# Kernel optimization log

Measured on AMD Instinct MI355X. Metric: run time of the kernel, lower is better.

Reference implementation:

```python
import jax, jax.numpy as jnp
import numpy as np

N_QUBITS = 8
DIM = 1 << N_QUBITS  # 256
PI = float(np.pi)

# Computational-basis bit signs: s_i = +1 for bit 0, -1 for bit 1 (Z eigenvalues).
# PennyLane convention: wire 0 is the most-significant bit.
_bits = (np.arange(DIM)[:, None] >> (N_QUBITS - 1 - np.arange(N_QUBITS))[None, :]) & 1
SIGNS = jnp.asarray(1.0 - 2.0 * _bits, dtype=jnp.float32)  # [DIM, 8]
PAIR_SIGNS = SIGNS[:, :-1] * SIGNS[:, 1:]                  # [DIM, 7]


def _mlp(x, W1, b1, W2, b2, W3, b3):
    h = jax.nn.relu(x @ W1.T + b1)
    h = jax.nn.relu(h @ W2.T + b2)
    return h @ W3.T + b3


def _embed_state(x):
    """QuantumEmbedding1 (ZZ feature map, IQP-style) on |0>^8.

    H on every wire, RZ(x_i) on wire i, then for i in 0..6:
    CNOT(i,i+1); RZ((pi-x_i)(pi-x_{i+1}), wire i+1); CNOT(i,i+1).
    The whole post-Hadamard circuit is diagonal, so the statevector has
    closed form: psi_b = 2^{-4} exp(-i/2 * phi(b)).
    x: [B, 8] -> psi: [B, 256] complex64.
    """
    single = x @ SIGNS.T                                    # [B, DIM]
    zz = (PI - x[:, :-1]) * (PI - x[:, 1:])                 # [B, 7]
    phase = single + zz @ PAIR_SIGNS.T                      # [B, DIM]
    return jnp.exp(-0.5j * phase) / 16.0                    # complex64


def _mean_rho(psi):
    B = psi.shape[0]
    return jnp.einsum('bi,bj->ij', psi, jnp.conj(psi)) / B  # [256, 256]


def setup_inputs() -> dict:
    key = jax.random.key(0)
    ks = jax.random.split(key, 8)
    B = 65536
    inp = {
        'x1': jax.random.normal(ks[0], (B, 8), dtype=jnp.float32),
        'x0': jax.random.normal(ks[1], (B, 8), dtype=jnp.float32),
        'W1': jax.random.normal(ks[2], (10, 8), dtype=jnp.float32) / np.sqrt(8.0),
        'b1': jnp.zeros((10,), dtype=jnp.float32),
        'W2': jax.random.normal(ks[3], (10, 10), dtype=jnp.float32) / np.sqrt(10.0),
        'b2': jnp.zeros((10,), dtype=jnp.float32),
        'W3': jax.random.normal(ks[4], (8, 10), dtype=jnp.float32) / np.sqrt(10.0),
        'b3': jnp.zeros((8,), dtype=jnp.float32),
    }
    return inp


def reference(x1, x0, W1, b1, W2, b2, W3, b3):
    h1 = _mlp(x1, W1, b1, W2, b2, W3, b3)
    h0 = _mlp(x0, W1, b1, W2, b2, W3, b3)
    rho1 = _mean_rho(_embed_state(h1))
    rho0 = _mean_rho(_embed_state(h0))
    rho_diff = rho1 - rho0
    rho_diff = 0.5 * (rho_diff + jnp.conj(rho_diff.T))  # exact Hermitian
    eigvals = jnp.linalg.eigvalsh(rho_diff)             # real eigenvalues
    return -0.5 * jnp.sum(jnp.abs(eigvals))
```

## Files before the change

### kernel.cpp

```cpp
#include <hip/hip_runtime.h>
#include <cstdint>
#include <cstddef>
#include <utility>

#define PI_F 3.14159265358979323846f

typedef __attribute__((ext_vector_type(8))) _Float16 half8;
typedef __attribute__((ext_vector_type(4))) float f32x4;

struct U4 { unsigned int w[4]; };

static __device__ __forceinline__ unsigned int packhalf2(float c, float s) {
  _Float16 hc = (_Float16)c, hs = (_Float16)s;
  unsigned short uc = __builtin_bit_cast(unsigned short, hc);
  unsigned short us = __builtin_bit_cast(unsigned short, hs);
  return (unsigned int)uc | ((unsigned int)us << 16);
}

static __device__ __forceinline__ void load16_lds(const void* g, void* l) {
  __builtin_amdgcn_global_load_lds(
      (const __attribute__((address_space(1))) unsigned int*)g,
      (__attribute__((address_space(3))) unsigned int*)l, 16, 0, 0);
}

__global__ __launch_bounds__(256) void k_mlp(
    const float* __restrict__ x1, const float* __restrict__ x0,
    const float* __restrict__ W1, const float* __restrict__ b1,
    const float* __restrict__ W2, const float* __restrict__ b2,
    const float* __restrict__ W3, const float* __restrict__ b3,
    float* __restrict__ hz, int B, float* __restrict__ scalars,
    float* __restrict__ out) {
  int s = blockIdx.x * blockDim.x + threadIdx.x;
  if (blockIdx.x == 0 && threadIdx.x == 0) {
    scalars[0] = 0.f;
    scalars[1] = 0.f;
    out[0] = 0.f;
  }
  if (s >= 2 * B) return;
  const float* xp = (s < B) ? (x1 + (size_t)s * 8) : (x0 + (size_t)(s - B) * 8);
  float x[8];
#pragma unroll
  for (int k = 0; k < 8; k++) x[k] = xp[k];
  float a1[10];
#pragma unroll
  for (int o = 0; o < 10; o++) {
    float v = b1[o];
#pragma unroll
    for (int k = 0; k < 8; k++) v = fmaf(W1[o * 8 + k], x[k], v);
    a1[o] = fmaxf(v, 0.f);
  }
  float a2[10];
#pragma unroll
  for (int o = 0; o < 10; o++) {
    float v = b2[o];
#pragma unroll
    for (int k = 0; k < 10; k++) v = fmaf(W2[o * 10 + k], a1[k], v);
    a2[o] = fmaxf(v, 0.f);
  }
  float h[8];
#pragma unroll
  for (int o = 0; o < 8; o++) {
    float v = b3[o];
#pragma unroll
    for (int k = 0; k < 10; k++) v = fmaf(W3[o * 10 + k], a2[k], v);
    h[o] = v;
  }
  float outv[16];
#pragma unroll
  for (int k = 0; k < 8; k++) outv[k] = h[k];
#pragma unroll
  for (int k = 0; k < 7; k++) outv[8 + k] = (PI_F - h[k]) * (PI_F - h[k + 1]);
  outv[15] = 0.f;
  float4* dst = (float4*)(hz + (size_t)s * 16);
#pragma unroll
  for (int q = 0; q < 4; q++) dst[q] = ((float4*)outv)[q];
}

__global__ __launch_bounds__(256) void k_gen(const float* __restrict__ hz,
                                             _Float16* __restrict__ Ach) {
  __shared__ float hzl[32][17];
  int kb = blockIdx.x, t = threadIdx.x;
  if (t < 128) {
    int smp = t >> 2, q = t & 3;
    const float4 v =
        *(const float4*)(hz + (size_t)(kb * 32 + smp) * 16 + q * 4);
    hzl[smp][q * 4 + 0] = v.x;
    hzl[smp][q * 4 + 1] = v.y;
    hzl[smp][q * 4 + 2] = v.z;
    hzl[smp][q * 4 + 3] = v.w;
  }
  __syncthreads();
  int s = t & 31, oct = t >> 5;
  float h[8], z[7];
#pragma unroll
  for (int k = 0; k < 8; k++) h[k] = hzl[s][k];
#pragma unroll
  for (int k = 0; k < 7; k++) z[k] = hzl[s][8 + k];
  float S5 = (oct & 4) ? -1.f : 1.f;
  float S6 = (oct & 2) ? -1.f : 1.f;
  float S7 = (oct & 1) ? -1.f : 1.f;
  float sg[5] = {1.f, 1.f, 1.f, 1.f, 1.f};
  float phi = h[0] + h[1] + h[2] + h[3] + h[4] + S5 * h[5] + S6 * h[6] +
              S7 * h[7] + z[0] + z[1] + z[2] + z[3] + S5 * z[4] +
              S5 * S6 * z[5] + S6 * S7 * z[6];
  _Float16* dst = Ach + (size_t)kb * 16384;
  const int halfoff = (2 * s) ^ (oct << 3);

  auto emit = [&](int g, float ph) {
    float r = ph * 0.07957747154594767f;
    r = r - floorf(r);
    float sv = __builtin_amdgcn_sinf(r);
    float cv = __builtin_amdgcn_cosf(r);
    *(unsigned int*)(dst + (size_t)(g * 8 + oct) * 64 + halfoff) =
        packhalf2(cv, sv);
  };

  emit(0, phi);
#pragma unroll
  for (int jj = 1; jj < 32; ++jj) {
    const int b = __builtin_ctz(jj);
    const int w = 4 - b;
    float nbl = (w == 0) ? 0.f : sg[w - 1] * z[w - 1];
    float nbr = (w == 4) ? S5 * z[4] : sg[w + 1] * z[w];
    phi -= 2.f * sg[w] * (h[w] + nbl + nbr);
    sg[w] = -sg[w];
    emit(jj ^ (jj >> 1), phi);
  }
}

#define ZSLABS 256

__global__ __launch_bounds__(256) void k_gemm(const _Float16* __restrict__ A,
                                              float* __restrict__ P,
                                              int kbPer) {
  __shared__ _Float16 lds[2][2][128][64];
  int bx = blockIdx.x, z = blockIdx.y;
  bool diag = (bx < 2);
  int mbase = (bx == 2) ? 0 : bx * 128;
  int nbase = (bx == 0) ? 0 : 128;
  int tile = (bx == 2) ? 1 : bx * 2;
  int bp = diag ? 0 : 1;
  int t = threadIdx.x, wave = t >> 6, lane = t & 63;
  int wm = wave >> 1, wn = wave & 1;
  unsigned int reMask = (z < ZSLABS / 2) ? 0u : 0x80008000u;
  unsigned int imMask = (z < ZSLABS / 2) ? 0x80000000u : 0x00008000u;
  int kb0 = z * kbPer;

  auto stage = [&](int it, int buf) {
    size_t kb = (size_t)(kb0 + it);
    const char* gA = (const char*)A + kb * 32768 + (size_t)mbase * 128;
    char* lA = (char*)&lds[buf][0][0][0];
#pragma unroll
    for (int q = 0; q < 4; q++) {
      int woff = wave * 4096 + q * 1024;
      load16_lds(gA + woff + lane * 16, lA + woff);
    }
    if (!diag) {
      const char* gB = (const char*)A + kb * 32768 + (size_t)nbase * 128;
      char* lB = (char*)&lds[buf][1][0][0];
#pragma unroll
      for (int q = 0; q < 4; q++) {
        int woff = wave * 4096 + q * 1024;
        load16_lds(gB + woff + lane * 16, lB + woff);
      }
    }
  };

  f32x4 accR[4][4] = {};
  f32x4 accI[4][4] = {};
  stage(0, 0);
  for (int it = 0; it < kbPer; ++it) {
    __syncthreads();
    if (it + 1 < kbPer) stage(it + 1, (it + 1) & 1);
    int buf = it & 1;
#pragma unroll
    for (int kk = 0; kk < 2; kk++) {
      int cbase = kk * 4 + (lane >> 4);
      half8 af[4], bfr[4], bfi[4];
#pragma unroll
      for (int fm = 0; fm < 4; fm++) {
        int r = wm * 64 + fm * 16 + (lane & 15);
        af[fm] = *(const half8*)&lds[buf][0][r][(cbase ^ (r & 7)) << 3];
      }
#pragma unroll
      for (int fn = 0; fn < 4; fn++) {
        int r = wn * 64 + fn * 16 + (lane & 15);
        half8 bv = *(const half8*)&lds[buf][bp][r][(cbase ^ (r & 7)) << 3];
        U4 u = __builtin_bit_cast(U4, bv), ur, ui;
#pragma unroll
        for (int q = 0; q < 4; q++) {
          unsigned int xv = u.w[q];
          ur.w[q] = xv ^ reMask;
          ui.w[q] = ((xv << 16) | (xv >> 16)) ^ imMask;
        }
        bfr[fn] = __builtin_bit_cast(half8, ur);
        bfi[fn] = __builtin_bit_cast(half8, ui);
      }
#pragma unroll
      for (int fm = 0; fm < 4; fm++)
#pragma unroll
        for (int fn = 0; fn < 4; fn++) {
          accR[fm][fn] = __builtin_amdgcn_mfma_f32_16x16x32_f16(
              af[fm], bfr[fn], accR[fm][fn], 0, 0, 0);
          accI[fm][fn] = __builtin_amdgcn_mfma_f32_16x16x32_f16(
              af[fm], bfi[fn], accI[fm][fn], 0, 0, 0);
        }
    }
  }
  float* PR = P + ((size_t)(tile * ZSLABS + z) * 2) * 16384;
  float* PI = PR + 16384;
  int r4 = (lane >> 4) * 4, cj = lane & 15;
#pragma unroll
  for (int fm = 0; fm < 4; fm++)
#pragma unroll
    for (int fn = 0; fn < 4; fn++)
#pragma unroll
      for (int r = 0; r < 4; r++) {
        int li = wm * 64 + fm * 16 + r4 + r;
        int lj = wn * 64 + fn * 16 + cj;
        PR[li * 128 + lj] = accR[fm][fn][r];
        PI[li * 128 + lj] = accI[fm][fn][r];
      }
}

__global__ __launch_bounds__(128) void k_reduce1(const float* __restrict__ P,
                                                 float* __restrict__ Q) {
  int r = blockIdx.x, tile = blockIdx.y, g = blockIdx.z, c = threadIdx.x;
  const float* base =
      P + ((size_t)(tile * ZSLABS + g * 32) * 2) * 16384 + r * 128 + c;
  float vR = 0.f, vI = 0.f;
  for (int u = 0; u < 32; u++) {
    vR += base[(size_t)u * 32768];
    vI += base[(size_t)u * 32768 + 16384];
  }
  size_t qidx = ((size_t)(g * 3 + tile) * 128 + r) * 128 + c;
  Q[qidx] = vR;
  Q[qidx + (size_t)8 * 3 * 16384] = vI;
}

__global__ __launch_bounds__(128) void k_reduce2(const float* __restrict__ Q,
                                                 float* __restrict__ AR,
                                                 float* __restrict__ AI,
                                                 float* __restrict__ sumsq,
                                                 float scale) {
  int r = blockIdx.x, tile = blockIdx.y, c = threadIdx.x;
  float vR = 0.f, vI = 0.f;
#pragma unroll
  for (int g = 0; g < 8; g++) {
    size_t qidx = ((size_t)(g * 3 + tile) * 128 + r) * 128 + c;
    vR += Q[qidx];
    vI += Q[qidx + (size_t)8 * 3 * 16384];
  }
  vR *= scale;
  vI *= scale;
  int i = (tile == 2) ? 128 + r : r;
  int j = (tile == 0) ? c : 128 + c;
  float ss = 0.f;
  bool diagTile = (tile != 1);
  if (!diagTile || c > r) {
    AR[i * 256 + j] = vR;
    AR[j * 256 + i] = vR;
    AI[i * 256 + j] = vI;
    AI[j * 256 + i] = -vI;
    ss = 2.f * (vR * vR + vI * vI);
  } else if (c == r) {
    AR[i * 256 + j] = vR;
    AI[i * 256 + j] = 0.f;
    ss = vR * vR;
  }
#pragma unroll
  for (int o = 32; o > 0; o >>= 1) ss += __shfl_down(ss, o);
  __shared__ float w2[2];
  if ((c & 63) == 0) w2[c >> 6] = ss;
  __syncthreads();
  if (c == 0) atomicAdd(sumsq, w2[0] + w2[1]);
}

__global__ __launch_bounds__(1024) void k_csq(
    const float* __restrict__ XR, const float* __restrict__ XI,
    float* __restrict__ YR, float* __restrict__ YI,
    float* __restrict__ sumsqY, int accumNorm) {
  __shared__ float rp[16][256][2];
  __shared__ float cpT[16][258][2];
  __shared__ float pacc[3][256][2];
  __shared__ float w16[16];
  int t = threadIdx.x;
  int bi = blockIdx.x >> 4, bj = blockIdx.x & 15;
  {
    int r = t >> 6, c = (t & 63) * 4;
    const float4 vr = *(const float4*)&XR[(bi * 16 + r) * 256 + c];
    const float4 vi = *(const float4*)&XI[(bi * 16 + r) * 256 + c];
    rp[r][c + 0][0] = vr.x; rp[r][c + 1][0] = vr.y;
    rp[r][c + 2][0] = vr.z; rp[r][c + 3][0] = vr.w;
    rp[r][c + 0][1] = vi.x; rp[r][c + 1][1] = vi.y;
    rp[r][c + 2][1] = vi.z; rp[r][c + 3][1] = vi.w;
    int row = t >> 2, c0 = (t & 3) * 4;
    const float4 wr = *(const float4*)&XR[row * 256 + bj * 16 + c0];
    const float4 wi = *(const float4*)&XI[row * 256 + bj * 16 + c0];
    cpT[c0 + 0][row][0] = wr.x; cpT[c0 + 1][row][0] = wr.y;
    cpT[c0 + 2][row][0] = wr.z; cpT[c0 + 3][row][0] = wr.w;
    cpT[c0 + 0][row][1] = wi.x; cpT[c0 + 1][row][1] = wi.y;
    cpT[c0 + 2][row][1] = wi.z; cpT[c0 + 3][row][1] = wi.w;
  }
  __syncthreads();
  int sub = t >> 8, tt = t & 255, ty = tt >> 4, tx = tt & 15;
  float sR = 0.f, sI = 0.f;
  int k0 = sub * 64;
#pragma unroll 8
  for (int k = k0; k < k0 + 64; k++) {
    float xr = rp[ty][k][0], xi = rp[ty][k][1];
    float yr = cpT[tx][k][0], yi = cpT[tx][k][1];
    sR = fmaf(xr, yr, sR);
    sR = fmaf(-xi, yi, sR);
    sI = fmaf(xr, yi, sI);
    sI = fmaf(xi, yr, sI);
  }
  if (sub) {
    pacc[sub - 1][tt][0] = sR;
    pacc[sub - 1][tt][1] = sI;
  }
  __syncthreads();
  float v = 0.f;
  if (sub == 0) {
    sR += (pacc[0][tt][0] + pacc[1][tt][0]) + pacc[2][tt][0];
    sI += (pacc[0][tt][1] + pacc[1][tt][1]) + pacc[2][tt][1];
    int i = bi * 16 + ty, j = bj * 16 + tx;
    YR[i * 256 + j] = sR;
    YI[i * 256 + j] = sI;
    if (accumNorm) v = sR * sR + sI * sI;
  }
#pragma unroll
  for (int o = 32; o > 0; o >>= 1) v += __shfl_down(v, o);
  if ((t & 63) == 0) w16[t >> 6] = v;
  __syncthreads();
  if (t == 0 && accumNorm)
    atomicAdd(sumsqY, (w16[0] + w16[1]) + (w16[2] + w16[3]));
}

__global__ __launch_bounds__(1024) void k_cupd(
    const float* __restrict__ XR, const float* __restrict__ XI,
    const float* __restrict__ YR, const float* __restrict__ YI,
    float* __restrict__ ZR, float* __restrict__ ZI,
    const float* __restrict__ scalars, int mode,
    const float* __restrict__ AR, const float* __restrict__ AI,
    float* __restrict__ out, int finalTrace) {
  __shared__ float rp[16][256][2];
  __shared__ float cpT[16][258][2];
  __shared__ float pacc[3][256][2];
  __shared__ float w16[16];
  int t = threadIdx.x;
  int bi = blockIdx.x >> 4, bj = blockIdx.x & 15;
  {
    int r = t >> 6, c = (t & 63) * 4;
    const float4 vr = *(const float4*)&XR[(bi * 16 + r) * 256 + c];
    const float4 vi = *(const float4*)&XI[(bi * 16 + r) * 256 + c];
    rp[r][c + 0][0] = vr.x; rp[r][c + 1][0] = vr.y;
    rp[r][c + 2][0] = vr.z; rp[r][c + 3][0] = vr.w;
    rp[r][c + 0][1] = vi.x; rp[r][c + 1][1] = vi.y;
    rp[r][c + 2][1] = vi.z; rp[r][c + 3][1] = vi.w;
    int row = t >> 2, c0 = (t & 3) * 4;
    const float4 wr = *(const float4*)&YR[row * 256 + bj * 16 + c0];
    const float4 wi = *(const float4*)&YI[row * 256 + bj * 16 + c0];
    cpT[c0 + 0][row][0] = wr.x; cpT[c0 + 1][row][0] = wr.y;
    cpT[c0 + 2][row][0] = wr.z; cpT[c0 + 3][row][0] = wr.w;
    cpT[c0 + 0][row][1] = wi.x; cpT[c0 + 1][row][1] = wi.y;
    cpT[c0 + 2][row][1] = wi.z; cpT[c0 + 3][row][1] = wi.w;
  }
  __syncthreads();
  int sub = t >> 8, tt = t & 255, ty = tt >> 4, tx = tt & 15;
  float sR = 0.f, sI = 0.f;
  int k0 = sub * 64;
#pragma unroll 8
  for (int k = k0; k < k0 + 64; k++) {
    float xr = rp[ty][k][0], xi = rp[ty][k][1];
    float yr = cpT[tx][k][0], yi = cpT[tx][k][1];
    sR = fmaf(xr, yr, sR);
    sR = fmaf(-xi, yi, sR);
    sI = fmaf(xr, yi, sI);
    sI = fmaf(xi, yr, sI);
  }
  if (sub) {
    pacc[sub - 1][tt][0] = sR;
    pacc[sub - 1][tt][1] = sI;
  }
  __syncthreads();
  float v = 0.f;
  if (sub == 0) {
    sR += (pacc[0][tt][0] + pacc[1][tt][0]) + pacc[2][tt][0];
    sI += (pacc[0][tt][1] + pacc[1][tt][1]) + pacc[2][tt][1];
    float aC, bC;
    if (mode == 0) {
      float f2 = scalars[0];
      float f = sqrtf(f2);
      float Rhat = 1.41421356f * sqrtf(scalars[1]) / f2;
      float g = 1.0f / (1.75f * Rhat);
      aC = 1.5f * g / f;
      float gf = g / f;
      bC = 0.5f * gf * gf * gf;
    } else if (mode == 1) {
      aC = 2.0f;
      bC = 1.0f;
    } else {
      aC = 1.5f;
      bC = 0.5f;
    }
    int idx = (bi * 16 + ty) * 256 + bj * 16 + tx;
    float zr = aC * XR[idx] - bC * sR;
    float zi = aC * XI[idx] - bC * sI;
    if (!finalTrace) {
      ZR[idx] = zr;
      ZI[idx] = zi;
    } else {
      v = AR[idx] * zr + AI[idx] * zi;
    }
  }
#pragma unroll
  for (int o = 32; o > 0; o >>= 1) v += __shfl_down(v, o);
  if ((t & 63) == 0) w16[t >> 6] = v;
  __syncthreads();
  if (t == 0 && finalTrace)
    atomicAdd(out, -0.5f * ((w16[0] + w16[1]) + (w16[2] + w16[3])));
}

extern "C" void kernel_launch(void* const* d_in, const int* in_sizes, int n_in,
                              void* d_out, int out_size, void* d_ws,
                              size_t ws_size, hipStream_t stream) {
  const float* x1 = (const float*)d_in[0];
  const float* x0 = (const float*)d_in[1];
  const float* W1 = (const float*)d_in[2];
  const float* b1 = (const float*)d_in[3];
  const float* W2 = (const float*)d_in[4];
  const float* b2 = (const float*)d_in[5];
  const float* W3 = (const float*)d_in[6];
  const float* b3 = (const float*)d_in[7];
  (void)n_in;
  (void)out_size;
  (void)ws_size;

  const int B = in_sizes[0] / 8;
  const int total = 2 * B;
  const int totalKb = total / 32;
  const int kbPer = totalKb / ZSLABS;

  char* ws = (char*)d_ws;
  size_t off = 0;
  auto carve = [&](size_t bytes) -> void* {
    off = (off + 255) & ~(size_t)255;
    void* p = ws + off;
    off += bytes;
    return p;
  };
  float* hz = (float*)carve((size_t)total * 16 * 4);
  _Float16* Ach = (_Float16*)carve((size_t)totalKb * 16384 * 2);
  float* P = (float*)carve((size_t)3 * ZSLABS * 2 * 16384 * 4);
  float* Q = (float*)carve((size_t)2 * 8 * 3 * 16384 * 4);
  float* scalars = (float*)carve(256);
  float* AR = (float*)carve(256 * 256 * 4);
  float* AI = (float*)carve(256 * 256 * 4);
  float* XR = (float*)carve(256 * 256 * 4);
  float* XI = (float*)carve(256 * 256 * 4);
  float* YR = (float*)carve(256 * 256 * 4);
  float* YI = (float*)carve(256 * 256 * 4);
  float* ZR = (float*)carve(256 * 256 * 4);
  float* ZI = (float*)carve(256 * 256 * 4);

  k_mlp<<<(total + 255) / 256, 256, 0, stream>>>(
      x1, x0, W1, b1, W2, b2, W3, b3, hz, B, scalars, (float*)d_out);
  k_gen<<<totalKb, 256, 0, stream>>>(hz, Ach);
  k_gemm<<<dim3(3, ZSLABS), 256, 0, stream>>>(Ach, P, kbPer);
  k_reduce1<<<dim3(128, 3, 8), 128, 0, stream>>>(P, Q);
  k_reduce2<<<dim3(128, 3), 128, 0, stream>>>(Q, AR, AI, scalars,
                                              1.0f / (256.0f * (float)B));

  const int NIT = 11;
  float *cR = AR, *cI = AI, *nR = XR, *nI = XI;
  for (int it = 0; it < NIT; it++) {
    int mode = (it == 0) ? 0 : (it <= 6 ? 1 : 2);
    int fin = (it == NIT - 1) ? 1 : 0;
    k_csq<<<256, 1024, 0, stream>>>(cR, cI, YR, YI, scalars + 1, it == 0);
    k_cupd<<<256, 1024, 0, stream>>>(cR, cI, YR, YI, nR, nI, scalars, mode, AR,
                                     AI, (float*)d_out, fin);
    if (it == 0) {
      cR = XR; cI = XI; nR = ZR; nI = ZI;
    } else {
      std::swap(cR, nR);
      std::swap(cI, nI);
    }
  }
}
```

Before: 264.8 us.

## Fuse Newton-Schulz iterations into one cooperative persistent kernel with grid sync

Replaces the 22 separate k_csq/k_cupd launches of the 11-iteration Newton-Schulz sign loop with a single cooperative kernel. The kernel runs all iterations and separates the dependent phases with grid.sync(). It also reuses the row panel already staged in shared memory for the aC*X term instead of re-reading X from global. The aim is to remove per-launch overhead and gaps between launches. In exchange it adds grid-wide barrier costs and requires all 256 blocks of 1024 threads to be co-resident.

New measurement: 896.6 us. 239% more time.

```diff
diff --git a/kernel.cpp b/kernel.cpp
--- a/kernel.cpp
+++ b/kernel.cpp
@@ -1,7 +1,10 @@
 #include <hip/hip_runtime.h>
+#include <hip/hip_cooperative_groups.h>
 #include <cstdint>
 #include <cstddef>
 #include <utility>
+
+namespace cg = cooperative_groups;
 
 #define PI_F 3.14159265358979323846f
 
@@ -276,119 +279,93 @@
   if (c == 0) atomicAdd(sumsq, w2[0] + w2[1]);
 }
 
-__global__ __launch_bounds__(1024) void k_csq(
-    const float* __restrict__ XR, const float* __restrict__ XI,
-    float* __restrict__ YR, float* __restrict__ YI,
-    float* __restrict__ sumsqY, int accumNorm) {
+__global__ __launch_bounds__(1024) void k_ns(
+    const float* AR, const float* AI, float* XR, float* XI, float* YR,
+    float* YI, float* ZR, float* ZI, float* scalars, float* out, int NIT) {
+  cg::grid_group grid = cg::this_grid();
   __shared__ float rp[16][256][2];
   __shared__ float cpT[16][258][2];
   __shared__ float pacc[3][256][2];
   __shared__ float w16[16];
-  int t = threadIdx.x;
-  int bi = blockIdx.x >> 4, bj = blockIdx.x & 15;
-  {
-    int r = t >> 6, c = (t & 63) * 4;
-    const float4 vr = *(const float4*)&XR[(bi * 16 + r) * 256 + c];
-    const float4 vi = *(const float4*)&XI[(bi * 16 + r) * 256 + c];
-    rp[r][c + 0][0] = vr.x; rp[r][c + 1][0] = vr.y;
-    rp[r][c + 2][0] = vr.z; rp[r][c + 3][0] = vr.w;
-    rp[r][c + 0][1] = vi.x; rp[r][c + 1][1] = vi.y;
-    rp[r][c + 2][1] = vi.z; rp[r][c + 3][1] = vi.w;
-    int row = t >> 2, c0 = (t & 3) * 4;
-    const float4 wr = *(const float4*)&XR[row * 256 + bj * 16 + c0];
-    const float4 wi = *(const float4*)&XI[row * 256 + bj * 16 + c0];
-    cpT[c0 + 0][row][0] = wr.x; cpT[c0 + 1][row][0] = wr.y;
-    cpT[c0 + 2][row][0] = wr.z; cpT[c0 + 3][row][0] = wr.w;
-    cpT[c0 + 0][row][1] = wi.x; cpT[c0 + 1][row][1] = wi.y;
-    cpT[c0 + 2][row][1] = wi.z; cpT[c0 + 3][row][1] = wi.w;
-  }
-  __syncthreads();
-  int sub = t >> 8, tt = t & 255, ty = tt >> 4, tx = tt & 15;
-  float sR = 0.f, sI = 0.f;
-  int k0 = sub * 64;
+  const int t = threadIdx.x;
+  const int bi = blockIdx.x >> 4, bj = blockIdx.x & 15;
+  const int sub = t >> 8, tt = t & 255, ty = tt >> 4, tx = tt & 15;
+  const int idx = (bi * 16 + ty) * 256 + bj * 16 + tx;
+
+  auto MM = [&](const float* LRr, const float* LIi, const float* RRr,
+                const float* RIi, float& sR, float& sI) {
+    __syncthreads();
+    {
+      int r = t >> 6, c = (t & 63) * 4;
+      const float4 vr = *(const float4*)&LRr[(bi * 16 + r) * 256 + c];
+      const float4 vi = *(const float4*)&LIi[(bi * 16 + r) * 256 + c];
+      rp[r][c + 0][0] = vr.x; rp[r][c + 1][0] = vr.y;
+      rp[r][c + 2][0] = vr.z; rp[r][c + 3][0] = vr.w;
+      rp[r][c + 0][1] = vi.x; rp[r][c + 1][1] = vi.y;
+      rp[r][c + 2][1] = vi.z; rp[r][c + 3][1] = vi.w;
+      int row = t >> 2, c0 = (t & 3) * 4;
+      const float4 wr = *(const float4*)&RRr[row * 256 + bj * 16 + c0];
+      const float4 wi = *(const float4*)&RIi[row * 256 + bj * 16 + c0];
+      cpT[c0 + 0][row][0] = wr.x; cpT[c0 + 1][row][0] = wr.y;
+      cpT[c0 + 2][row][0] = wr.z; cpT[c0 + 3][row][0] = wr.w;
+      cpT[c0 + 0][row][1] = wi.x; cpT[c0 + 1][row][1] = wi.y;
+      cpT[c0 + 2][row][1] = wi.z; cpT[c0 + 3][row][1] = wi.w;
+    }
+    __syncthreads();
+    sR = 0.f;
+    sI = 0.f;
+    int k0 = sub * 64;
 #pragma unroll 8
-  for (int k = k0; k < k0 + 64; k++) {
-    float xr = rp[ty][k][0], xi = rp[ty][k][1];
-    float yr = cpT[tx][k][0], yi = cpT[tx][k][1];
-    sR = fmaf(xr, yr, sR);
-    sR = fmaf(-xi, yi, sR);
-    sI = fmaf(xr, yi, sI);
-    sI = fmaf(xi, yr, sI);
-  }
-  if (sub) {
-    pacc[sub - 1][tt][0] = sR;
-    pacc[sub - 1][tt][1] = sI;
-  }
-  __syncthreads();
-  float v = 0.f;
-  if (sub == 0) {
-    sR += (pacc[0][tt][0] + pacc[1][tt][0]) + pacc[2][tt][0];
-    sI += (pacc[0][tt][1] + pacc[1][tt][1]) + pacc[2][tt][1];
-    int i = bi * 16 + ty, j = bj * 16 + tx;
-    YR[i * 256 + j] = sR;
-    YI[i * 256 + j] = sI;
-    if (accumNorm) v = sR * sR + sI * sI;
-  }
-#pragma unroll
-  for (int o = 32; o > 0; o >>= 1) v += __shfl_down(v, o);
-  if ((t & 63) == 0) w16[t >> 6] = v;
-  __syncthreads();
-  if (t == 0 && accumNorm)
-    atomicAdd(sumsqY, (w16[0] + w16[1]) + (w16[2] + w16[3]));
-}
-
-__global__ __launch_bounds__(1024) void k_cupd(
-    const float* __restrict__ XR, const float* __restrict__ XI,
-    const float* __restrict__ YR, const float* __restrict__ YI,
-    float* __restrict__ ZR, float* __restrict__ ZI,
-    const float* __restrict__ scalars, int mode,
-    const float* __restrict__ AR, const float* __restrict__ AI,
-    float* __restrict__ out, int finalTrace) {
-  __shared__ float rp[16][256][2];
-  __shared__ float cpT[16][258][2];
-  __shared__ float pacc[3][256][2];
-  __shared__ float w16[16];
-  int t = threadIdx.x;
-  int bi = blockIdx.x >> 4, bj = blockIdx.x & 15;
-  {
-    int r = t >> 6, c = (t & 63) * 4;
-    const float4 vr = *(const float4*)&XR[(bi * 16 + r) * 256 + c];
-    const float4 vi = *(const float4*)&XI[(bi * 16 + r) * 256 + c];
-    rp[r][c + 0][0] = vr.x; rp[r][c + 1][0] = vr.y;
-    rp[r][c + 2][0] = vr.z; rp[r][c + 3][0] = vr.w;
-    rp[r][c + 0][1] = vi.x; rp[r][c + 1][1] = vi.y;
-    rp[r][c + 2][1] = vi.z; rp[r][c + 3][1] = vi.w;
-    int row = t >> 2, c0 = (t & 3) * 4;
-    const float4 wr = *(const float4*)&YR[row * 256 + bj * 16 + c0];
-    const float4 wi = *(const float4*)&YI[row * 256 + bj * 16 + c0];
-    cpT[c0 + 0][row][0] = wr.x; cpT[c0 + 1][row][0] = wr.y;
-    cpT[c0 + 2][row][0] = wr.z; cpT[c0 + 3][row][0] = wr.w;
-    cpT[c0 + 0][row][1] = wi.x; cpT[c0 + 1][row][1] = wi.y;
-    cpT[c0 + 2][row][1] = wi.z; cpT[c0 + 3][row][1] = wi.w;
-  }
-  __syncthreads();
-  int sub = t >> 8, tt = t & 255, ty = tt >> 4, tx = tt & 15;
-  float sR = 0.f, sI = 0.f;
-  int k0 = sub * 64;
-#pragma unroll 8
-  for (int k = k0; k < k0 + 64; k++) {
-    float xr = rp[ty][k][0], xi = rp[ty][k][1];
-    float yr = cpT[tx][k][0], yi = cpT[tx][k][1];
-    sR = fmaf(xr, yr, sR);
-    sR = fmaf(-xi, yi, sR);
-    sI = fmaf(xr, yi, sI);
-    sI = fmaf(xi, yr, sI);
-  }
-  if (sub) {
-    pacc[sub - 1][tt][0] = sR;
-    pacc[sub - 1][tt][1] = sI;
-  }
-  __syncthreads();
-  float v = 0.f;
-  if (sub == 0) {
-    sR += (pacc[0][tt][0] + pacc[1][tt][0]) + pacc[2][tt][0];
-    sI += (pacc[0][tt][1] + pacc[1][tt][1]) + pacc[2][tt][1];
+    for (int k = k0; k < k0 + 64; k++) {
+      float xr = rp[ty][k][0], xi = rp[ty][k][1];
+      float yr = cpT[tx][k][0], yi = cpT[tx][k][1];
+      sR = fmaf(xr, yr, sR);
+      sR = fmaf(-xi, yi, sR);
+      sI = fmaf(xr, yi, sI);
+      sI = fmaf(xi, yr, sI);
+    }
+    if (sub) {
+      pacc[sub - 1][tt][0] = sR;
+      pacc[sub - 1][tt][1] = sI;
+    }
+    __syncthreads();
+    if (sub == 0) {
+      sR += (pacc[0][tt][0] + pacc[1][tt][0]) + pacc[2][tt][0];
+      sI += (pacc[0][tt][1] + pacc[1][tt][1]) + pacc[2][tt][1];
+    }
+  };
+
+  auto blockAtomic = [&](float v, float* dst, float scale) {
+#pragma unroll
+    for (int o = 32; o > 0; o >>= 1) v += __shfl_down(v, o);
+    if ((t & 63) == 0) w16[t >> 6] = v;
+    __syncthreads();
+    if (t == 0) {
+      float s = 0.f;
+#pragma unroll
+      for (int q = 0; q < 16; q++) s += w16[q];
+      atomicAdd(dst, scale * s);
+    }
+  };
+
+  const float *cR = AR, *cI = AI;
+  float *nR = XR, *nI = XI;
+  for (int it = 0; it < NIT; ++it) {
+    float sR, sI;
+    MM(cR, cI, cR, cI, sR, sI);
+    if (sub == 0) {
+      YR[idx] = sR;
+      YI[idx] = sI;
+    }
+    if (it == 0) {
+      float v = (sub == 0) ? (sR * sR + sI * sI) : 0.f;
+      blockAtomic(v, scalars + 1, 1.0f);
+    }
+    grid.sync();
+    float mR, mI;
+    MM(cR, cI, YR, YI, mR, mI);
     float aC, bC;
+    int mode = (it == 0) ? 0 : (it <= 6 ? 1 : 2);
     if (mode == 0) {
       float f2 = scalars[0];
       float f = sqrtf(f2);
@@ -404,22 +381,29 @@
       aC = 1.5f;
       bC = 0.5f;
     }
-    int idx = (bi * 16 + ty) * 256 + bj * 16 + tx;
-    float zr = aC * XR[idx] - bC * sR;
-    float zi = aC * XI[idx] - bC * sI;
-    if (!finalTrace) {
-      ZR[idx] = zr;
-      ZI[idx] = zi;
+    if (it < NIT - 1) {
+      if (sub == 0) {
+        nR[idx] = aC * rp[ty][bj * 16 + tx][0] - bC * mR;
+        nI[idx] = aC * rp[ty][bj * 16 + tx][1] - bC * mI;
+      }
+      grid.sync();
     } else {
-      v = AR[idx] * zr + AI[idx] * zi;
-    }
-  }
-#pragma unroll
-  for (int o = 32; o > 0; o >>= 1) v += __shfl_down(v, o);
-  if ((t & 63) == 0) w16[t >> 6] = v;
-  __syncthreads();
-  if (t == 0 && finalTrace)
-    atomicAdd(out, -0.5f * ((w16[0] + w16[1]) + (w16[2] + w16[3])));
+      float v = 0.f;
+      if (sub == 0) {
+        float zr = aC * rp[ty][bj * 16 + tx][0] - bC * mR;
+        float zi = aC * rp[ty][bj * 16 + tx][1] - bC * mI;
+        v = AR[idx] * zr + AI[idx] * zi;
+      }
+      blockAtomic(v, out, -0.5f);
+    }
+    if (it == 0) {
+      cR = XR; cI = XI; nR = ZR; nI = ZI;
+    } else {
+      const float* tmpR = cR; const float* tmpI = cI;
+      cR = nR; cI = nI;
+      nR = (float*)tmpR; nI = (float*)tmpI;
+    }
+  }
 }
 
 extern "C" void kernel_launch(void* const* d_in, const int* in_sizes, int n_in,
@@ -472,19 +456,10 @@
   k_reduce2<<<dim3(128, 3), 128, 0, stream>>>(Q, AR, AI, scalars,
                                               1.0f / (256.0f * (float)B));
 
-  const int NIT = 11;
-  float *cR = AR, *cI = AI, *nR = XR, *nI = XI;
-  for (int it = 0; it < NIT; it++) {
-    int mode = (it == 0) ? 0 : (it <= 6 ? 1 : 2);
-    int fin = (it == NIT - 1) ? 1 : 0;
-    k_csq<<<256, 1024, 0, stream>>>(cR, cI, YR, YI, scalars + 1, it == 0);
-    k_cupd<<<256, 1024, 0, stream>>>(cR, cI, YR, YI, nR, nI, scalars, mode, AR,
-                                     AI, (float*)d_out, fin);
-    if (it == 0) {
-      cR = XR; cI = XI; nR = ZR; nI = ZI;
-    } else {
-      std::swap(cR, nR);
-      std::swap(cI, nI);
-    }
-  }
-}
+  int nit = 11;
+  float* outp = (float*)d_out;
+  void* args[] = {&AR, &AI, &XR, &XI, &YR, &YI,
+                  &ZR, &ZI, &scalars, &outp, &nit};
+  hipLaunchCooperativeKernel((void*)k_ns, dim3(256), dim3(1024), args, 0,
+                             stream);
+}
```

## Restructure Hermitian GEMM into 512 load-balanced blocks with 8 waves each

Applied to the files above, without the earlier changes.

The rho GEMM kernel is replaced by one that launches 512 blocks of 512 threads. Diagonal quadrant tiles get 128 blocks with 32 k-steps each and the off-diagonal tile gets 256 blocks with 16 k-steps, so per-block work is balanced. Each wave now computes a 32x64 sub-tile with a smaller accumulator set, which is meant to raise occupancy and spread work across more CUs than the previous 3x256 grid of 4-wave blocks. The hardcoded kb0<2048 sign split and fixed slab counts tie the kernel to the batch size B=65536, and the reduction kernels are updated to index the new partial layout.

Measured after the change: 253.0 us. -4.5%, faster.

```diff
diff --git a/kernel.cpp b/kernel.cpp
--- a/kernel.cpp
+++ b/kernel.cpp
@@ -128,46 +128,33 @@
   }
 }
 
-#define ZSLABS 256
-
-__global__ __launch_bounds__(256) void k_gemm(const _Float16* __restrict__ A,
-                                              float* __restrict__ P,
-                                              int kbPer) {
-  __shared__ _Float16 lds[2][2][128][64];
-  int bx = blockIdx.x, z = blockIdx.y;
-  bool diag = (bx < 2);
-  int mbase = (bx == 2) ? 0 : bx * 128;
-  int nbase = (bx == 0) ? 0 : 128;
-  int tile = (bx == 2) ? 1 : bx * 2;
-  int bp = diag ? 0 : 1;
+__global__ __launch_bounds__(512) void k_gemm_q(const _Float16* __restrict__ A,
+                                                float* __restrict__ P) {
+  __shared__ _Float16 lds[2][16384];
+  int b = blockIdx.x;
+  int qt = (b < 128) ? 0 : (b < 384 ? 1 : 2);
+  int z = b - ((qt == 0) ? 0 : (qt == 1) ? 128 : 384);
+  int kbPer = (qt == 1) ? 16 : 32;
+  int kb0 = z * kbPer;
+  int chunkOff = (qt == 2) ? 16384 : 0;
+  int bRowBase = (qt == 1) ? 128 : 0;
   int t = threadIdx.x, wave = t >> 6, lane = t & 63;
-  int wm = wave >> 1, wn = wave & 1;
-  unsigned int reMask = (z < ZSLABS / 2) ? 0u : 0x80008000u;
-  unsigned int imMask = (z < ZSLABS / 2) ? 0x80000000u : 0x00008000u;
-  int kb0 = z * kbPer;
+  unsigned int reMask = (kb0 < 2048) ? 0u : 0x80008000u;
+  unsigned int imMask = (kb0 < 2048) ? 0x80000000u : 0x00008000u;
 
   auto stage = [&](int it, int buf) {
-    size_t kb = (size_t)(kb0 + it);
-    const char* gA = (const char*)A + kb * 32768 + (size_t)mbase * 128;
-    char* lA = (char*)&lds[buf][0][0][0];
-#pragma unroll
-    for (int q = 0; q < 4; q++) {
-      int woff = wave * 4096 + q * 1024;
-      load16_lds(gA + woff + lane * 16, lA + woff);
-    }
-    if (!diag) {
-      const char* gB = (const char*)A + kb * 32768 + (size_t)nbase * 128;
-      char* lB = (char*)&lds[buf][1][0][0];
-#pragma unroll
-      for (int q = 0; q < 4; q++) {
-        int woff = wave * 4096 + q * 1024;
-        load16_lds(gB + woff + lane * 16, lB + woff);
-      }
+    const char* g = (const char*)A + (size_t)(kb0 + it) * 32768 + chunkOff;
+    char* l = (char*)&lds[buf][0];
+    load16_lds(g + t * 16, l + t * 16);
+    load16_lds(g + 8192 + t * 16, l + 8192 + t * 16);
+    if (qt == 1) {
+      load16_lds(g + 16384 + t * 16, l + 16384 + t * 16);
+      load16_lds(g + 24576 + t * 16, l + 24576 + t * 16);
     }
   };
 
-  f32x4 accR[4][4] = {};
-  f32x4 accI[4][4] = {};
+  f32x4 accR[2][4] = {};
+  f32x4 accI[2][4] = {};
   stage(0, 0);
   for (int it = 0; it < kbPer; ++it) {
     __syncthreads();
@@ -175,17 +162,17 @@
     int buf = it & 1;
 #pragma unroll
     for (int kk = 0; kk < 2; kk++) {
-      int cbase = kk * 4 + (lane >> 4);
-      half8 af[4], bfr[4], bfi[4];
-#pragma unroll
-      for (int fm = 0; fm < 4; fm++) {
-        int r = wm * 64 + fm * 16 + (lane & 15);
-        af[fm] = *(const half8*)&lds[buf][0][r][(cbase ^ (r & 7)) << 3];
+      int cb = kk * 4 + (lane >> 4);
+      half8 af[2];
+#pragma unroll
+      for (int fr = 0; fr < 2; fr++) {
+        int r = (wave >> 1) * 32 + fr * 16 + (lane & 15);
+        af[fr] = *(const half8*)&lds[buf][r * 64 + ((cb ^ (r & 7)) << 3)];
       }
 #pragma unroll
-      for (int fn = 0; fn < 4; fn++) {
-        int r = wn * 64 + fn * 16 + (lane & 15);
-        half8 bv = *(const half8*)&lds[buf][bp][r][(cbase ^ (r & 7)) << 3];
+      for (int fc = 0; fc < 4; fc++) {
+        int rb = bRowBase + (wave & 1) * 64 + fc * 16 + (lane & 15);
+        half8 bv = *(const half8*)&lds[buf][rb * 64 + ((cb ^ (rb & 7)) << 3)];
         U4 u = __builtin_bit_cast(U4, bv), ur, ui;
 #pragma unroll
         for (int q = 0; q < 4; q++) {
@@ -193,47 +180,46 @@
           ur.w[q] = xv ^ reMask;
           ui.w[q] = ((xv << 16) | (xv >> 16)) ^ imMask;
         }
-        bfr[fn] = __builtin_bit_cast(half8, ur);
-        bfi[fn] = __builtin_bit_cast(half8, ui);
+        half8 bfr = __builtin_bit_cast(half8, ur);
+        half8 bfi = __builtin_bit_cast(half8, ui);
+#pragma unroll
+        for (int fr = 0; fr < 2; fr++) {
+          accR[fr][fc] = __builtin_amdgcn_mfma_f32_16x16x32_f16(
+              af[fr], bfr, accR[fr][fc], 0, 0, 0);
+          accI[fr][fc] = __builtin_amdgcn_mfma_f32_16x16x32_f16(
+              af[fr], bfi, accI[fr][fc], 0, 0, 0);
+        }
       }
-#pragma unroll
-      for (int fm = 0; fm < 4; fm++)
-#pragma unroll
-        for (int fn = 0; fn < 4; fn++) {
-          accR[fm][fn] = __builtin_amdgcn_mfma_f32_16x16x32_f16(
-              af[fm], bfr[fn], accR[fm][fn], 0, 0, 0);
-          accI[fm][fn] = __builtin_amdgcn_mfma_f32_16x16x32_f16(
-              af[fm], bfi[fn], accI[fm][fn], 0, 0, 0);
-        }
     }
   }
-  float* PR = P + ((size_t)(tile * ZSLABS + z) * 2) * 16384;
+  float* PR = P + (size_t)b * 32768;
   float* PI = PR + 16384;
   int r4 = (lane >> 4) * 4, cj = lane & 15;
 #pragma unroll
-  for (int fm = 0; fm < 4; fm++)
-#pragma unroll
-    for (int fn = 0; fn < 4; fn++)
+  for (int fr = 0; fr < 2; fr++)
+#pragma unroll
+    for (int fc = 0; fc < 4; fc++)
 #pragma unroll
       for (int r = 0; r < 4; r++) {
-        int li = wm * 64 + fm * 16 + r4 + r;
-        int lj = wn * 64 + fn * 16 + cj;
-        PR[li * 128 + lj] = accR[fm][fn][r];
-        PI[li * 128 + lj] = accI[fm][fn][r];
+        int li = (wave >> 1) * 32 + fr * 16 + r4 + r;
+        int lj = (wave & 1) * 64 + fc * 16 + cj;
+        PR[li * 128 + lj] = accR[fr][fc][r];
+        PI[li * 128 + lj] = accI[fr][fc][r];
       }
 }
 
 __global__ __launch_bounds__(128) void k_reduce1(const float* __restrict__ P,
                                                  float* __restrict__ Q) {
-  int r = blockIdx.x, tile = blockIdx.y, g = blockIdx.z, c = threadIdx.x;
-  const float* base =
-      P + ((size_t)(tile * ZSLABS + g * 32) * 2) * 16384 + r * 128 + c;
+  int r = blockIdx.x, qt = blockIdx.y, g = blockIdx.z, c = threadIdx.x;
+  int nsl = (qt == 1) ? 32 : 16;
+  int b0 = ((qt == 0) ? 0 : (qt == 1) ? 128 : 384) + g * nsl;
   float vR = 0.f, vI = 0.f;
-  for (int u = 0; u < 32; u++) {
-    vR += base[(size_t)u * 32768];
-    vI += base[(size_t)u * 32768 + 16384];
-  }
-  size_t qidx = ((size_t)(g * 3 + tile) * 128 + r) * 128 + c;
+  for (int u = 0; u < nsl; u++) {
+    const float* base = P + (size_t)(b0 + u) * 32768 + r * 128 + c;
+    vR += base[0];
+    vI += base[16384];
+  }
+  size_t qidx = ((size_t)(g * 3 + qt) * 128 + r) * 128 + c;
   Q[qidx] = vR;
   Q[qidx + (size_t)8 * 3 * 16384] = vI;
 }
@@ -243,21 +229,21 @@
                                                  float* __restrict__ AI,
                                                  float* __restrict__ sumsq,
                                                  float scale) {
-  int r = blockIdx.x, tile = blockIdx.y, c = threadIdx.x;
+  int r = blockIdx.x, qt = blockIdx.y, c = threadIdx.x;
   float vR = 0.f, vI = 0.f;
 #pragma unroll
   for (int g = 0; g < 8; g++) {
-    size_t qidx = ((size_t)(g * 3 + tile) * 128 + r) * 128 + c;
+    size_t qidx = ((size_t)(g * 3 + qt) * 128 + r) * 128 + c;
     vR += Q[qidx];
     vI += Q[qidx + (size_t)8 * 3 * 16384];
   }
   vR *= scale;
   vI *= scale;
-  int i = (tile == 2) ? 128 + r : r;
-  int j = (tile == 0) ? c : 128 + c;
+  int i = (qt == 2) ? 128 + r : r;
+  int j = (qt == 0) ? c : 128 + c;
   float ss = 0.f;
-  bool diagTile = (tile != 1);
-  if (!diagTile || c > r) {
+  bool diagQ = (qt != 1);
+  if (!diagQ || c > r) {
     AR[i * 256 + j] = vR;
     AR[j * 256 + i] = vR;
     AI[i * 256 + j] = vI;
@@ -440,7 +426,6 @@
   const int B = in_sizes[0] / 8;
   const int total = 2 * B;
   const int totalKb = total / 32;
-  const int kbPer = totalKb / ZSLABS;
 
   char* ws = (char*)d_ws;
   size_t off = 0;
@@ -452,7 +437,7 @@
   };
   float* hz = (float*)carve((size_t)total * 16 * 4);
   _Float16* Ach = (_Float16*)carve((size_t)totalKb * 16384 * 2);
-  float* P = (float*)carve((size_t)3 * ZSLABS * 2 * 16384 * 4);
+  float* P = (float*)carve((size_t)512 * 32768 * 4);
   float* Q = (float*)carve((size_t)2 * 8 * 3 * 16384 * 4);
   float* scalars = (float*)carve(256);
   float* AR = (float*)carve(256 * 256 * 4);
@@ -467,7 +452,7 @@
   k_mlp<<<(total + 255) / 256, 256, 0, stream>>>(
       x1, x0, W1, b1, W2, b2, W3, b3, hz, B, scalars, (float*)d_out);
   k_gen<<<totalKb, 256, 0, stream>>>(hz, Ach);
-  k_gemm<<<dim3(3, ZSLABS), 256, 0, stream>>>(Ach, P, kbPer);
+  k_gemm_q<<<512, 512, 0, stream>>>(Ach, P);
   k_reduce1<<<dim3(128, 3, 8), 128, 0, stream>>>(P, Q);
   k_reduce2<<<dim3(128, 3), 128, 0, stream>>>(Q, AR, AI, scalars,
                                               1.0f / (256.0f * (float)B));
```
